# Optimization experiments

Hardware: AMD Instinct MI355X
Metric: run time of the kernel (lower is better)

The kernel has to match this reference:

```python
import jax, jax.numpy as jnp
import numpy as np
from jax import lax

HEADS = 8
C, H, W = 64, 16, 16
D_K = C // HEADS
SCALE = 1.0 / np.sqrt(D_K * H * W).astype(np.float32)


def conv2d(x, w, b):
    # x: [N, C, H, W], w: [O, I, 3, 3], padding=1
    y = lax.conv_general_dilated(x, w, window_strides=(1, 1),
                                 padding=((1, 1), (1, 1)),
                                 dimension_numbers=('NCHW', 'OIHW', 'NCHW'))
    return y + b[None, :, None, None]


def _project(x, w, b, bs, seq):
    # x: [bs, seq, C, H, W] -> conv per frame -> [bs, heads, seq, d_k*H*W]
    y = conv2d(x.reshape(bs * seq, C, H, W), w, b)
    y = y.reshape(bs, seq, HEADS, D_K, H, W)
    y = jnp.transpose(y, (0, 2, 1, 3, 4, 5)).reshape(bs, HEADS, seq, D_K * H * W)
    return y


def setup_inputs() -> dict:
    key = jax.random.key(0)
    ks = jax.random.split(key, 11)
    shp = (2, 256, C, H, W)
    wstd = 1.0 / np.sqrt(C * 9)  # torch Conv2d default init scale
    inp = {
        'q': jax.random.normal(ks[0], shp, jnp.float32),
        'k': jax.random.normal(ks[1], shp, jnp.float32),
        'v': jax.random.normal(ks[2], shp, jnp.float32),
        'Wq': jax.random.uniform(ks[3], (C, C, 3, 3), jnp.float32, -wstd, wstd),
        'bq': jax.random.uniform(ks[4], (C,), jnp.float32, -wstd, wstd),
        'Wk': jax.random.uniform(ks[5], (C, C, 3, 3), jnp.float32, -wstd, wstd),
        'bk': jax.random.uniform(ks[6], (C,), jnp.float32, -wstd, wstd),
        'Wv': jax.random.uniform(ks[7], (C, C, 3, 3), jnp.float32, -wstd, wstd),
        'bv': jax.random.uniform(ks[8], (C,), jnp.float32, -wstd, wstd),
        'Wo': jax.random.uniform(ks[9], (C, C, 3, 3), jnp.float32, -wstd, wstd),
        'bo': jax.random.uniform(ks[10], (C,), jnp.float32, -wstd, wstd),
    }
    return inp


def reference(q, k, v, Wq, bq, Wk, bk, Wv, bv, Wo, bo):
    bs, seq = q.shape[0], q.shape[1]
    qh = _project(q, Wq, bq, bs, seq)  # [bs, h, seq, d_k*H*W]
    kh = _project(k, Wk, bk, bs, seq)
    vh = _project(v, Wv, bv, bs, seq)
    scores = jnp.einsum('bhqd,bhkd->bhqk', qh, kh) * SCALE
    attn = jax.nn.softmax(scores, axis=-1)
    out = jnp.einsum('bhqk,bhkd->bhqd', attn, vh)  # [bs, h, seq, d_k*H*W]
    out = out.reshape(bs, HEADS, seq, D_K, H, W)
    concat = jnp.transpose(out, (0, 2, 1, 3, 4, 5)).reshape(bs * seq, C, H, W)
    y = conv2d(concat, Wo, bo).reshape(bs, seq, C, H, W)
    return y
```

## Files before the change

kernel.cpp:

```cpp
#include <hip/hip_runtime.h>
#include <hip/hip_bf16.h>
#include <hip/hip_fp16.h>

typedef unsigned short u16;
typedef _Float16 f16x8 __attribute__((ext_vector_type(8)));
typedef u16 u16x8 __attribute__((ext_vector_type(8)));
typedef u16 u16x4 __attribute__((ext_vector_type(4)));
typedef float f32x4 __attribute__((ext_vector_type(4)));

__device__ __forceinline__ u16 f2h(float f){
  __half h = __float2half(f);
  return *(u16*)&h;
}

__device__ __forceinline__ void cp16_async(const u16* g, u16* l){
  __builtin_amdgcn_global_load_lds(
      (const __attribute__((address_space(1))) unsigned int*)g,
      (__attribute__((address_space(3))) unsigned int*)l,
      16, 0, 0);
}

__device__ __forceinline__ void prep_w_body(const float* W, u16* Wt, int i){
  if (i >= 36864) return;
  int co = i / 576, rem = i % 576, ci = rem / 9, tap = rem % 9;
  int n = co >> 4, lr = co & 15, kk = ci >> 5, lg = (ci >> 3) & 3, j = ci & 7;
  int s = tap*2 + kk;
  Wt[(((s*4 + n)*64) + lg*16 + lr)*8 + j] = f2h(W[i]);
}

__global__ __launch_bounds__(256) void prep_w3(
    const float* __restrict__ Wq, const float* __restrict__ Wk,
    const float* __restrict__ Wv, u16* __restrict__ Wt)
{
  int which = blockIdx.y;
  const float* W = (which == 0) ? Wq : (which == 1) ? Wk : Wv;
  prep_w_body(W, Wt + which*36864, blockIdx.x * 256 + threadIdx.x);
}

__global__ __launch_bounds__(256) void prep_w(
    const float* __restrict__ W, u16* __restrict__ Wt)
{
  prep_w_body(W, Wt, blockIdx.x * 256 + threadIdx.x);
}

template<bool IN_F32, bool OUT_PROJ>
__device__ __forceinline__ void conv_body(
    const void* __restrict__ xin, const u16* __restrict__ Wt,
    const float* __restrict__ bias, void* __restrict__ dst,
    int frame, u16* xT, int tid)
{
  for (int i = tid; i < 2592; i += 256)
    *(uint4*)((char*)xT + i*16) = make_uint4(0u, 0u, 0u, 0u);
  __syncthreads();

  {
    const int p = tid, py = p >> 4, px = p & 15;
    const int pp = (py + 1)*18 + px + 1;
    const float* xf = (const float*)xin + (size_t)frame * 16384;
    const u16*   xb = (const u16*)  xin + (size_t)frame * 16384;
    #pragma unroll
    for (int cb = 0; cb < 8; ++cb){
      u16x8 pk;
      #pragma unroll
      for (int j = 0; j < 8; ++j){
        int ci = cb*8 + j;
        pk[j] = IN_F32 ? f2h(xf[ci*256 + p]) : xb[ci*256 + p];
      }
      unsigned off = (unsigned)(pp*128) + ((((unsigned)cb + (unsigned)pp) & 7u) << 4);
      *(u16x8*)((char*)xT + off) = pk;
    }
  }
  __syncthreads();

  const int w = tid >> 6, lane = tid & 63, lr = lane & 15, lg = lane >> 4;
  const int pyb = w * 4;

  f32x4 acc[4][4];
  #pragma unroll
  for (int n = 0; n < 4; ++n){
    float b = bias[n*16 + lr];
    #pragma unroll
    for (int m = 0; m < 4; ++m){
      acc[m][n][0] = b; acc[m][n][1] = b; acc[m][n][2] = b; acc[m][n][3] = b;
    }
  }

  #define LOADB(s, B) do {                                                  \
    _Pragma("unroll")                                                       \
    for (int n_ = 0; n_ < 4; ++n_)                                          \
      B[n_] = *(const f16x8*)(Wt + ((((s)*4 + n_)*64) + lane)*8);           \
  } while(0)

  #define STEP(s, B) do {                                                   \
    int tap_ = (s) >> 1, kk_ = (s) & 1;                                     \
    int dy_ = tap_ / 3, dx_ = tap_ - dy_*3;                                 \
    f16x8 af_[4];                                                           \
    _Pragma("unroll")                                                       \
    for (int m_ = 0; m_ < 4; ++m_){                                         \
      int pp_ = (pyb + m_ + dy_)*18 + lr + dx_;                             \
      unsigned slot_ = ((unsigned)(kk_*4 + lg) + (unsigned)pp_) & 7u;       \
      af_[m_] = *(const f16x8*)((const char*)xT                             \
                 + (unsigned)(pp_*128) + (slot_ << 4));                     \
    }                                                                       \
    _Pragma("unroll")                                                       \
    for (int m_ = 0; m_ < 4; ++m_)                                          \
      _Pragma("unroll")                                                     \
      for (int n_ = 0; n_ < 4; ++n_)                                        \
        acc[m_][n_] = __builtin_amdgcn_mfma_f32_16x16x32_f16(               \
            af_[m_], B[n_], acc[m_][n_], 0, 0, 0);                          \
  } while(0)

  f16x8 Ba[4], Bb[4];
  LOADB(0, Ba);
  #pragma unroll 1
  for (int it = 0; it < 9; ++it){
    LOADB(it*2 + 1, Bb);
    STEP(it*2, Ba);
    if (it < 8) LOADB(it*2 + 2, Ba);
    STEP(it*2 + 1, Bb);
  }
  #undef LOADB
  #undef STEP

  __syncthreads();
  char* xTc = (char*)xT;
  if (OUT_PROJ){
    #pragma unroll
    for (int n = 0; n < 4; ++n){
      int co = n*16 + lr;
      #pragma unroll
      for (int m = 0; m < 4; ++m){
        int px0 = w*64 + m*16 + lg*4;
        int s = px0 >> 3;
        unsigned aw = (unsigned)(co*512) + (unsigned)((s ^ (co & 7)) << 4)
                      + (unsigned)((px0 & 7) * 2);
        u16x4 o4;
        #pragma unroll
        for (int r = 0; r < 4; ++r) o4[r] = f2h(acc[m][n][r]);
        *(u16x4*)(xTc + aw) = o4;
      }
    }
    __syncthreads();
    u16* d = (u16*)dst;
    const int b = frame >> 8, sq = frame & 255;
    #pragma unroll
    for (int i = 0; i < 8; ++i){
      int c = w*8 + i;
      int co = c*2 + (lane >> 5);
      int pxo = (lane & 31) * 8;
      unsigned ld = (unsigned)(co*512) + (unsigned)(((lane & 31) ^ (co & 7)) << 4);
      uint4 v = *(const uint4*)(xTc + ld);
      int h = co >> 3, dk = co & 7;
      u16* gp = d + ((size_t)((b*8 + h)*256 + sq))*2048 + dk*256 + pxo;
      *(uint4*)gp = v;
    }
  } else {
    float* dfr = (float*)dst + (size_t)frame * 16384;
    #pragma unroll
    for (int ph2 = 0; ph2 < 2; ++ph2){
      if ((w >> 1) == ph2){
        #pragma unroll
        for (int n = 0; n < 4; ++n){
          int co = n*16 + lr;
          #pragma unroll
          for (int m = 0; m < 4; ++m){
            int pxl = (w & 1)*64 + m*16 + lg*4;
            int s = pxl >> 2;
            unsigned aw = (unsigned)(co*512) + (unsigned)((s ^ (co & 7)) << 4);
            *(f32x4*)(xTc + aw) = acc[m][n];
          }
        }
      }
      __syncthreads();
      #pragma unroll
      for (int i = 0; i < 8; ++i){
        int c = w*8 + i;
        int co = c*2 + (lane >> 5);
        int pxl = (lane & 31) * 4;
        unsigned ld = (unsigned)(co*512) + (unsigned)(((lane & 31) ^ (co & 7)) << 4);
        f32x4 v = *(const f32x4*)(xTc + ld);
        *(f32x4*)(dfr + co*256 + ph2*128 + pxl) = v;
      }
      if (ph2 == 0) __syncthreads();
    }
  }
}

__global__ __launch_bounds__(256, 3) void conv3_mfma(
    const float* __restrict__ q, const float* __restrict__ k,
    const float* __restrict__ v, const u16* __restrict__ Wt3,
    const float* __restrict__ bq, const float* __restrict__ bk,
    const float* __restrict__ bv,
    u16* __restrict__ qh, u16* __restrict__ kh, u16* __restrict__ vh)
{
  __shared__ __align__(16) u16 xT[324 * 64];
  const int which = blockIdx.x >> 9;
  const int frame = blockIdx.x & 511;
  const float* x = (which == 0) ? q : (which == 1) ? k : v;
  const float* bias = (which == 0) ? bq : (which == 1) ? bk : bv;
  u16* dst = (which == 0) ? qh : (which == 1) ? kh : vh;
  conv_body<true, true>(x, Wt3 + which*36864, bias, dst, frame, xT, threadIdx.x);
}

__global__ __launch_bounds__(256, 3) void conv_out_mfma(
    const u16* __restrict__ xin, const u16* __restrict__ Wt,
    const float* __restrict__ bias, float* __restrict__ out)
{
  __shared__ __align__(16) u16 xT[324 * 64];
  conv_body<false, false>(xin, Wt, bias, out, blockIdx.x, xT, threadIdx.x);
}

__global__ __launch_bounds__(256) void transpose_v(
    const u16* __restrict__ vh, u16* __restrict__ vt)
{
  __shared__ u16 tile[64][72];
  const int tid = threadIdx.x;
  const int dt = blockIdx.x, st = blockIdx.y, bh = blockIdx.z;
  {
    int r = tid >> 2, c4 = tid & 3;
    const u16* src = vh + ((size_t)(bh*256 + st*64 + r))*2048 + dt*64 + c4*16;
    uint4 v0 = *(const uint4*)src;
    uint4 v1 = *(const uint4*)(src + 8);
    *(uint4*)&tile[r][c4*16]     = v0;
    *(uint4*)&tile[r][c4*16 + 8] = v1;
  }
  __syncthreads();
  {
    int dr = tid >> 2, s4 = tid & 3;
    u16 tmp[16];
    #pragma unroll
    for (int i = 0; i < 16; ++i) tmp[i] = tile[s4*16 + i][dr];
    u16* dstp = vt + ((size_t)(bh*2048 + dt*64 + dr))*256 + st*64 + s4*16;
    *(uint4*)dstp       = *(uint4*)&tmp[0];
    *(uint4*)(dstp + 8) = *(uint4*)&tmp[8];
  }
}

__global__ __launch_bounds__(512, 2) void attn_kernel(
    const u16* __restrict__ qh, const u16* __restrict__ kh,
    const u16* __restrict__ vt, u16* __restrict__ obuf)
{
  const float SCALE = 0.022097086912079608f;
  __shared__ __align__(16) u16 Qs[16*2048];
  __shared__ __align__(16) u16 Kb[2][16384];
  __shared__ __align__(16) u16 P[16*256];
  __shared__ float redA[8][16];
  __shared__ float redB[8][16];

  const int tid = threadIdx.x;
  const int w = tid >> 6, lane = tid & 63, lr = lane & 15, lg = lane >> 4;

  const int id = blockIdx.x;
  const int xcd = id & 7, j = id >> 3;
  const int bh = xcd + 8*(j & 1), qt = j >> 1;
  const int q0 = qt * 16, b = bh >> 3, h = bh & 7;

  const u16* Qg = qh + ((size_t)(bh*256 + q0))*2048;
  const u16* Kg = kh + (size_t)bh * 256 * 2048;
  const u16* Vg = vt + (size_t)bh * 2048 * 256;

  const int spK = (lane & 7) ^ ((lane >> 3) & 7);
  #define STAGE_K(c, buf)                                                   \
    _Pragma("unroll")                                                       \
    for (int r_ = 0; r_ < 4; ++r_)                                          \
      cp16_async(Kg + (size_t)(w*32 + r_*8 + (lane>>3))*2048 + (c)*64 + spK*8, \
                 (buf) + w*2048 + r_*512);

  #define STAGE_V(c, buf)                                                   \
    _Pragma("unroll")                                                       \
    for (int r_ = 0; r_ < 8; ++r_){                                         \
      int rl_ = w*16 + r_*2 + (lane>>5);                                    \
      int sp_ = (lane & 31) ^ (rl_ & 7);                                    \
      cp16_async(Vg + (size_t)((c)*128 + rl_)*256 + sp_*8,                  \
                 (buf) + w*4096 + r_*512);                                  \
    }

  #pragma unroll
  for (int r = 0; r < 8; ++r){
    int t = r*64 + lane;
    int row = w*2 + (t >> 8);
    int dp = t & 255;
    int sp = (dp & ~7) | ((dp & 7) ^ (row & 7));
    cp16_async(Qg + (size_t)row*2048 + sp*8, Qs + w*4096 + r*512);
  }
  STAGE_K(0, Kb[0]);
  __syncthreads();

  const f32x4 zero4 = {0.f, 0.f, 0.f, 0.f};
  f32x4 sacc[2] = {zero4, zero4};
  #pragma unroll 1
  for (int c = 0; c < 32; ++c){
    if (c < 31) STAGE_K(c+1, Kb[(c+1)&1]);
    const u16* kb = Kb[c&1];
    #pragma unroll
    for (int d2 = 0; d2 < 2; ++d2){
      unsigned aoff = (((unsigned)lr << 12) + (unsigned)(c*128 + d2*64 + lg*16))
                      ^ (unsigned)((lr & 7) << 4);
      f16x8 a = *(const f16x8*)((const char*)Qs + aoff);
      #pragma unroll
      for (int n = 0; n < 2; ++n){
        int row = w*32 + n*16 + lr;
        const u16* kp = kb + row*64 + (((d2*4 + lg) ^ (row & 7)) << 3);
        f16x8 bk = *(const f16x8*)kp;
        sacc[n] = __builtin_amdgcn_mfma_f32_16x16x32_f16(a, bk, sacc[n], 0,0,0);
      }
    }
    __syncthreads();
  }

  float mx[4];
  #pragma unroll
  for (int r = 0; r < 4; ++r){
    float vv = fmaxf(sacc[0][r], sacc[1][r]);
    #pragma unroll
    for (int off = 1; off < 16; off <<= 1) vv = fmaxf(vv, __shfl_xor(vv, off));
    mx[r] = vv;
  }
  if (lr == 0){
    #pragma unroll
    for (int r = 0; r < 4; ++r) redA[w][lg*4 + r] = mx[r];
  }
  __syncthreads();
  #pragma unroll
  for (int r = 0; r < 4; ++r){
    int row = lg*4 + r;
    float vv = redA[0][row];
    #pragma unroll
    for (int ww = 1; ww < 8; ++ww) vv = fmaxf(vv, redA[ww][row]);
    mx[r] = vv;
  }

  const int kbase = w * 32;
  float sm[4] = {0.f, 0.f, 0.f, 0.f};
  #pragma unroll
  for (int n = 0; n < 2; ++n)
    #pragma unroll
    for (int r = 0; r < 4; ++r){
      float pv = __expf((sacc[n][r] - mx[r]) * SCALE);
      sm[r] += pv;
      int row = lg*4 + r;
      int col = kbase + n*16 + lr;
      unsigned off = (((unsigned)row << 9) + ((unsigned)col << 1))
                     ^ (unsigned)((row & 7) << 4);
      *(u16*)((char*)P + off) = f2h(pv);
    }
  #pragma unroll
  for (int r = 0; r < 4; ++r){
    float vv = sm[r];
    #pragma unroll
    for (int off = 1; off < 16; off <<= 1) vv += __shfl_xor(vv, off);
    sm[r] = vv;
  }
  if (lr == 0){
    #pragma unroll
    for (int r = 0; r < 4; ++r) redB[w][lg*4 + r] = sm[r];
  }
  __syncthreads();
  float rs[4];
  #pragma unroll
  for (int r = 0; r < 4; ++r){
    int row = lg*4 + r;
    float s = redB[0][row];
    #pragma unroll
    for (int ww = 1; ww < 8; ++ww) s += redB[ww][row];
    rs[r] = 1.0f / s;
  }

  u16* Vb0 = Qs;
  u16* Vb1 = &Kb[0][0];
  STAGE_V(0, Vb0);
  __syncthreads();
  #pragma unroll 1
  for (int c = 0; c < 16; ++c){
    if (c < 15){
      u16* nbuf = ((c+1) & 1) ? Vb1 : Vb0;
      STAGE_V(c+1, nbuf);
    }
    const u16* vb = (c & 1) ? Vb1 : Vb0;
    f32x4 oacc = zero4;
    #pragma unroll
    for (int kt = 0; kt < 8; ++kt){
      unsigned poff = (((unsigned)lr << 9) + (unsigned)(kt*64 + lg*16))
                      ^ (unsigned)((lr & 7) << 4);
      f16x8 pa = *(const f16x8*)((const char*)P + poff);
      int row = w*16 + lr;
      const u16* vp = vb + row*256 + (((kt*4 + lg) ^ (row & 7)) << 3);
      f16x8 bv = *(const f16x8*)vp;
      oacc = __builtin_amdgcn_mfma_f32_16x16x32_f16(pa, bv, oacc, 0,0,0);
    }
    #pragma unroll
    for (int r = 0; r < 4; ++r){
      float o = oacc[r] * rs[r];
      int qrow = q0 + lg*4 + r;
      int d = c*128 + w*16 + lr;
      int frame = b*256 + qrow;
      int cdim = h*8 + (d >> 8);
      obuf[((size_t)(frame*64 + cdim))*256 + (d & 255)] = f2h(o);
    }
    __syncthreads();
  }
  #undef STAGE_K
  #undef STAGE_V
}

extern "C" void kernel_launch(void* const* d_in, const int* in_sizes, int n_in,
                              void* d_out, int out_size, void* d_ws, size_t ws_size,
                              hipStream_t stream)
{
  const float* q  = (const float*)d_in[0];
  const float* k  = (const float*)d_in[1];
  const float* v  = (const float*)d_in[2];
  const float* Wq = (const float*)d_in[3];
  const float* bq = (const float*)d_in[4];
  const float* Wk = (const float*)d_in[5];
  const float* bk = (const float*)d_in[6];
  const float* Wv = (const float*)d_in[7];
  const float* bv = (const float*)d_in[8];
  const float* Wo = (const float*)d_in[9];
  const float* bo = (const float*)d_in[10];
  float* out = (float*)d_out;

  char* ws = (char*)d_ws;
  u16* qh = (u16*)(ws);
  u16* kh = (u16*)(ws + (size_t)16*1024*1024);
  u16* vh = (u16*)(ws + (size_t)32*1024*1024);
  u16* vt = (u16*)(ws + (size_t)48*1024*1024);
  u16* obuf = vh;
  u16* Wt3  = vt;
  u16* WtO  = qh;

  prep_w3<<<dim3(144, 3), dim3(256), 0, stream>>>(Wq, Wk, Wv, Wt3);
  conv3_mfma<<<dim3(1536), dim3(256), 0, stream>>>(q, k, v, Wt3, bq, bk, bv,
                                                   qh, kh, vh);
  transpose_v<<<dim3(32, 4, 16), dim3(256), 0, stream>>>(vh, vt);
  attn_kernel<<<dim3(256), dim3(512), 0, stream>>>(qh, kh, vt, obuf);
  prep_w<<<dim3(144), dim3(256), 0, stream>>>(Wo, WtO);
  conv_out_mfma<<<dim3(512), dim3(256), 0, stream>>>(obuf, WtO, bo, out);
}
```

Measured before the change: 115.6 us.

## Warp-specialize conv kernels with double-buffered LDS staging across multiple frames

Replaces the one-frame-per-block conv kernels with a persistent 512-thread kernel. Four staging waves load and convert the next frame's input into a second LDS buffer while four compute waves run MFMA on the current frame. Each block handles F frames (6 for the QKV projection, 2 for the output conv), so global-load latency is hidden behind compute. In exchange, LDS per block doubles, half the waves do no MFMA, and the grid shrinks to 256 blocks, which may reduce parallelism across CUs.

```diff
diff --git a/kernel.cpp b/kernel.cpp
--- a/kernel.cpp
+++ b/kernel.cpp
@@ -43,55 +43,79 @@
   prep_w_body(W, Wt, blockIdx.x * 256 + threadIdx.x);
 }
 
-template<bool IN_F32, bool OUT_PROJ>
-__device__ __forceinline__ void conv_body(
-    const void* __restrict__ xin, const u16* __restrict__ Wt,
-    const float* __restrict__ bias, void* __restrict__ dst,
-    int frame, u16* xT, int tid)
+template<bool IN_F32, bool OUT_PROJ, int F>
+__global__ __launch_bounds__(512, 2) void conv_pipe(
+    const void* __restrict__ x0, const void* __restrict__ x1,
+    const void* __restrict__ x2, const u16* __restrict__ Wt_base,
+    int wt_stride, const float* __restrict__ b0,
+    const float* __restrict__ b1, const float* __restrict__ b2,
+    void* __restrict__ d0, void* __restrict__ d1, void* __restrict__ d2)
 {
-  for (int i = tid; i < 2592; i += 256)
-    *(uint4*)((char*)xT + i*16) = make_uint4(0u, 0u, 0u, 0u);
-  __syncthreads();
-
-  {
-    const int p = tid, py = p >> 4, px = p & 15;
-    const int pp = (py + 1)*18 + px + 1;
-    const float* xf = (const float*)xin + (size_t)frame * 16384;
-    const u16*   xb = (const u16*)  xin + (size_t)frame * 16384;
-    #pragma unroll
-    for (int cb = 0; cb < 8; ++cb){
-      u16x8 pk;
-      #pragma unroll
-      for (int j = 0; j < 8; ++j){
-        int ci = cb*8 + j;
-        pk[j] = IN_F32 ? f2h(xf[ci*256 + p]) : xb[ci*256 + p];
-      }
-      unsigned off = (unsigned)(pp*128) + ((((unsigned)cb + (unsigned)pp) & 7u) << 4);
-      *(u16x8*)((char*)xT + off) = pk;
-    }
-  }
-  __syncthreads();
-
+  __shared__ __align__(16) u16 xT0[324*64];
+  __shared__ __align__(16) u16 xT1[324*64];
+  const int tid = threadIdx.x;
   const int w = tid >> 6, lane = tid & 63, lr = lane & 15, lg = lane >> 4;
+  const bool stagew = (w >= 4);
+  const int sp = tid & 255;
+  const int spy = sp >> 4, spx = sp & 15;
+  const int spp = (spy + 1)*18 + spx + 1;
+  const int gf0 = blockIdx.x * F;
   const int pyb = w * 4;
 
-  f32x4 acc[4][4];
-  #pragma unroll
-  for (int n = 0; n < 4; ++n){
-    float b = bias[n*16 + lr];
-    #pragma unroll
-    for (int m = 0; m < 4; ++m){
-      acc[m][n][0] = b; acc[m][n][1] = b; acc[m][n][2] = b; acc[m][n][3] = b;
-    }
-  }
-
-  #define LOADB(s, B) do {                                                  \
+  u16x8 pk[8];
+
+  #define LOADCVT(gf) do {                                                  \
+    int wh_ = (gf) >> 9, fr_ = (gf) & 511;                                  \
+    const void* xs_ = (wh_==0)?x0:(wh_==1)?x1:x2;                           \
+    if (IN_F32){                                                            \
+      const float* s_ = (const float*)xs_ + (size_t)fr_*16384;              \
+      float xv_[64];                                                        \
+      _Pragma("unroll") for (int c=0;c<64;++c) xv_[c] = s_[c*256 + sp];     \
+      _Pragma("unroll") for (int cb=0;cb<8;++cb){                           \
+        u16x8 t_;                                                           \
+        _Pragma("unroll") for (int j=0;j<8;++j) t_[j] = f2h(xv_[cb*8+j]);   \
+        pk[cb] = t_;                                                        \
+      }                                                                     \
+    } else {                                                                \
+      const u16* s_ = (const u16*)xs_ + (size_t)fr_*16384;                  \
+      _Pragma("unroll") for (int cb=0;cb<8;++cb){                           \
+        u16x8 t_;                                                           \
+        _Pragma("unroll") for (int j=0;j<8;++j) t_[j] = s_[(cb*8+j)*256+sp];\
+        pk[cb] = t_;                                                        \
+      }                                                                     \
+    }                                                                       \
+    _Pragma("unroll") for (int cb=0;cb<8;++cb){                             \
+      unsigned* pw_ = (unsigned*)&pk[cb];                                   \
+      asm volatile("" :: "v"(pw_[0]), "v"(pw_[1]), "v"(pw_[2]), "v"(pw_[3]));\
+    }                                                                       \
+  } while(0)
+
+  #define PACKW(buf) do {                                                   \
+    _Pragma("unroll") for (int cb=0;cb<8;++cb){                             \
+      unsigned off_ = (unsigned)(spp*128)                                   \
+                      + ((((unsigned)cb + (unsigned)spp) & 7u) << 4);       \
+      *(u16x8*)((char*)(buf) + off_) = pk[cb];                              \
+    }                                                                       \
+  } while(0)
+
+  #define ZPAD(buf) do {                                                    \
+    for (int i_ = sp; i_ < 544; i_ += 256){                                 \
+      int r_ = i_ >> 3, q_ = i_ & 7, row_;                                  \
+      if (r_ < 18)      row_ = r_;                                          \
+      else if (r_ < 34) row_ = 18*(r_ - 17);                                \
+      else if (r_ < 50) row_ = 18*(r_ - 33) + 17;                           \
+      else              row_ = 306 + (r_ - 50);                             \
+      *(uint4*)((char*)(buf) + row_*128 + q_*16) = make_uint4(0u,0u,0u,0u); \
+    }                                                                       \
+  } while(0)
+
+  #define LOADB(s, B, Wt) do {                                              \
     _Pragma("unroll")                                                       \
     for (int n_ = 0; n_ < 4; ++n_)                                          \
-      B[n_] = *(const f16x8*)(Wt + ((((s)*4 + n_)*64) + lane)*8);           \
+      B[n_] = *(const f16x8*)((Wt) + ((((s)*4 + n_)*64) + lane)*8);         \
   } while(0)
 
-  #define STEP(s, B) do {                                                   \
+  #define STEP(s, B, buf) do {                                              \
     int tap_ = (s) >> 1, kk_ = (s) & 1;                                     \
     int dy_ = tap_ / 3, dx_ = tap_ - dy_*3;                                 \
     f16x8 af_[4];                                                           \
@@ -99,7 +123,7 @@
     for (int m_ = 0; m_ < 4; ++m_){                                         \
       int pp_ = (pyb + m_ + dy_)*18 + lr + dx_;                             \
       unsigned slot_ = ((unsigned)(kk_*4 + lg) + (unsigned)pp_) & 7u;       \
-      af_[m_] = *(const f16x8*)((const char*)xT                             \
+      af_[m_] = *(const f16x8*)((const char*)(buf)                          \
                  + (unsigned)(pp_*128) + (slot_ << 4));                     \
     }                                                                       \
     _Pragma("unroll")                                                       \
@@ -110,55 +134,89 @@
             af_[m_], B[n_], acc[m_][n_], 0, 0, 0);                          \
   } while(0)
 
-  f16x8 Ba[4], Bb[4];
-  LOADB(0, Ba);
+  if (stagew) LOADCVT(gf0);
+  for (int i = tid; i < 2592; i += 512){
+    *(uint4*)((char*)xT0 + i*16) = make_uint4(0u,0u,0u,0u);
+    *(uint4*)((char*)xT1 + i*16) = make_uint4(0u,0u,0u,0u);
+  }
+  __syncthreads();
+  if (stagew) PACKW(xT0);
+  __syncthreads();
+
   #pragma unroll 1
-  for (int it = 0; it < 9; ++it){
-    LOADB(it*2 + 1, Bb);
-    STEP(it*2, Ba);
-    if (it < 8) LOADB(it*2 + 2, Ba);
-    STEP(it*2 + 1, Bb);
-  }
-  #undef LOADB
-  #undef STEP
-
-  __syncthreads();
-  char* xTc = (char*)xT;
-  if (OUT_PROJ){
-    #pragma unroll
-    for (int n = 0; n < 4; ++n){
-      int co = n*16 + lr;
+  for (int f = 0; f < F; ++f){
+    const int gf = gf0 + f;
+    const int wh = gf >> 9, frame = gf & 511;
+    const u16* Wt = Wt_base + wh*wt_stride;
+    const float* bias = (wh==0)?b0:(wh==1)?b1:b2;
+    u16* cur = (f & 1) ? xT1 : xT0;
+    u16* nxt = (f & 1) ? xT0 : xT1;
+
+    if (stagew && f + 1 < F) LOADCVT(gf + 1);
+
+    f32x4 acc[4][4];
+    if (!stagew){
       #pragma unroll
-      for (int m = 0; m < 4; ++m){
-        int px0 = w*64 + m*16 + lg*4;
-        int s = px0 >> 3;
-        unsigned aw = (unsigned)(co*512) + (unsigned)((s ^ (co & 7)) << 4)
-                      + (unsigned)((px0 & 7) * 2);
-        u16x4 o4;
-        #pragma unroll
-        for (int r = 0; r < 4; ++r) o4[r] = f2h(acc[m][n][r]);
-        *(u16x4*)(xTc + aw) = o4;
+      for (int n = 0; n < 4; ++n){
+        float b = bias[n*16 + lr];
+        #pragma unroll
+        for (int m = 0; m < 4; ++m){
+          acc[m][n][0] = b; acc[m][n][1] = b; acc[m][n][2] = b; acc[m][n][3] = b;
+        }
+      }
+      f16x8 Ba[4], Bb[4];
+      LOADB(0, Ba, Wt);
+      #pragma unroll 1
+      for (int it = 0; it < 9; ++it){
+        LOADB(it*2 + 1, Bb, Wt);
+        STEP(it*2, Ba, cur);
+        if (it < 8) LOADB(it*2 + 2, Ba, Wt);
+        STEP(it*2 + 1, Bb, cur);
       }
     }
     __syncthreads();
-    u16* d = (u16*)dst;
-    const int b = frame >> 8, sq = frame & 255;
-    #pragma unroll
-    for (int i = 0; i < 8; ++i){
-      int c = w*8 + i;
-      int co = c*2 + (lane >> 5);
-      int pxo = (lane & 31) * 8;
-      unsigned ld = (unsigned)(co*512) + (unsigned)(((lane & 31) ^ (co & 7)) << 4);
-      uint4 v = *(const uint4*)(xTc + ld);
-      int h = co >> 3, dk = co & 7;
-      u16* gp = d + ((size_t)((b*8 + h)*256 + sq))*2048 + dk*256 + pxo;
-      *(uint4*)gp = v;
-    }
-  } else {
-    float* dfr = (float*)dst + (size_t)frame * 16384;
-    #pragma unroll
-    for (int ph2 = 0; ph2 < 2; ++ph2){
-      if ((w >> 1) == ph2){
+
+    char* tc = (char*)cur;
+    if (OUT_PROJ){
+      if (!stagew){
+        #pragma unroll
+        for (int n = 0; n < 4; ++n){
+          int co = n*16 + lr;
+          #pragma unroll
+          for (int m = 0; m < 4; ++m){
+            int px0 = w*64 + m*16 + lg*4;
+            int s = px0 >> 3;
+            unsigned aw = (unsigned)(co*512) + (unsigned)((s ^ (co & 7)) << 4)
+                          + (unsigned)((px0 & 7) * 2);
+            u16x4 o4;
+            #pragma unroll
+            for (int r = 0; r < 4; ++r) o4[r] = f2h(acc[m][n][r]);
+            *(u16x4*)(tc + aw) = o4;
+          }
+        }
+      } else if (f + 1 < F){
+        ZPAD(nxt); PACKW(nxt);
+      }
+      __syncthreads();
+      if (!stagew){
+        u16* d = (u16*)((wh==0)?d0:(wh==1)?d1:d2);
+        const int b = frame >> 8, sq = frame & 255;
+        #pragma unroll
+        for (int i = 0; i < 8; ++i){
+          int c = w*8 + i;
+          int co = c*2 + (lane >> 5);
+          int pxo = (lane & 31) * 8;
+          unsigned ld = (unsigned)(co*512) + (unsigned)(((lane & 31) ^ (co & 7)) << 4);
+          uint4 v = *(const uint4*)(tc + ld);
+          int h = co >> 3, dk = co & 7;
+          u16* gp = d + ((size_t)((b*8 + h)*256 + sq))*2048 + dk*256 + pxo;
+          *(uint4*)gp = v;
+        }
+      }
+      __syncthreads();
+    } else {
+      float* dfr = (float*)d0 + (size_t)frame * 16384;
+      if (!stagew && (w >> 1) == 0){
         #pragma unroll
         for (int n = 0; n < 4; ++n){
           int co = n*16 + lr;
@@ -167,47 +225,57 @@
             int pxl = (w & 1)*64 + m*16 + lg*4;
             int s = pxl >> 2;
             unsigned aw = (unsigned)(co*512) + (unsigned)((s ^ (co & 7)) << 4);
-            *(f32x4*)(xTc + aw) = acc[m][n];
+            *(f32x4*)(tc + aw) = acc[m][n];
           }
         }
       }
+      if (stagew && f + 1 < F){ ZPAD(nxt); PACKW(nxt); }
       __syncthreads();
-      #pragma unroll
-      for (int i = 0; i < 8; ++i){
-        int c = w*8 + i;
-        int co = c*2 + (lane >> 5);
-        int pxl = (lane & 31) * 4;
-        unsigned ld = (unsigned)(co*512) + (unsigned)(((lane & 31) ^ (co & 7)) << 4);
-        f32x4 v = *(const f32x4*)(xTc + ld);
-        *(f32x4*)(dfr + co*256 + ph2*128 + pxl) = v;
-      }
-      if (ph2 == 0) __syncthreads();
-    }
-  }
-}
-
-__global__ __launch_bounds__(256, 3) void conv3_mfma(
-    const float* __restrict__ q, const float* __restrict__ k,
-    const float* __restrict__ v, const u16* __restrict__ Wt3,
-    const float* __restrict__ bq, const float* __restrict__ bk,
-    const float* __restrict__ bv,
-    u16* __restrict__ qh, u16* __restrict__ kh, u16* __restrict__ vh)
-{
-  __shared__ __align__(16) u16 xT[324 * 64];
-  const int which = blockIdx.x >> 9;
-  const int frame = blockIdx.x & 511;
-  const float* x = (which == 0) ? q : (which == 1) ? k : v;
-  const float* bias = (which == 0) ? bq : (which == 1) ? bk : bv;
-  u16* dst = (which == 0) ? qh : (which == 1) ? kh : vh;
-  conv_body<true, true>(x, Wt3 + which*36864, bias, dst, frame, xT, threadIdx.x);
-}
-
-__global__ __launch_bounds__(256, 3) void conv_out_mfma(
-    const u16* __restrict__ xin, const u16* __restrict__ Wt,
-    const float* __restrict__ bias, float* __restrict__ out)
-{
-  __shared__ __align__(16) u16 xT[324 * 64];
-  conv_body<false, false>(xin, Wt, bias, out, blockIdx.x, xT, threadIdx.x);
+      if (!stagew){
+        #pragma unroll
+        for (int i = 0; i < 8; ++i){
+          int c = w*8 + i;
+          int co = c*2 + (lane >> 5);
+          int pxl = (lane & 31) * 4;
+          unsigned ld = (unsigned)(co*512) + (unsigned)(((lane & 31) ^ (co & 7)) << 4);
+          f32x4 v = *(const f32x4*)(tc + ld);
+          *(f32x4*)(dfr + co*256 + pxl) = v;
+        }
+      }
+      __syncthreads();
+      if (!stagew && (w >> 1) == 1){
+        #pragma unroll
+        for (int n = 0; n < 4; ++n){
+          int co = n*16 + lr;
+          #pragma unroll
+          for (int m = 0; m < 4; ++m){
+            int pxl = (w & 1)*64 + m*16 + lg*4;
+            int s = pxl >> 2;
+            unsigned aw = (unsigned)(co*512) + (unsigned)((s ^ (co & 7)) << 4);
+            *(f32x4*)(tc + aw) = acc[m][n];
+          }
+        }
+      }
+      __syncthreads();
+      if (!stagew){
+        #pragma unroll
+        for (int i = 0; i < 8; ++i){
+          int c = w*8 + i;
+          int co = c*2 + (lane >> 5);
+          int pxl = (lane & 31) * 4;
+          unsigned ld = (unsigned)(co*512) + (unsigned)(((lane & 31) ^ (co & 7)) << 4);
+          f32x4 v = *(const f32x4*)(tc + ld);
+          *(f32x4*)(dfr + co*256 + 128 + pxl) = v;
+        }
+      }
+      __syncthreads();
+    }
+  }
+  #undef LOADCVT
+  #undef PACKW
+  #undef ZPAD
+  #undef LOADB
+  #undef STEP
 }
 
 __global__ __launch_bounds__(256) void transpose_v(
@@ -430,10 +498,11 @@
   u16* WtO  = qh;
 
   prep_w3<<<dim3(144, 3), dim3(256), 0, stream>>>(Wq, Wk, Wv, Wt3);
-  conv3_mfma<<<dim3(1536), dim3(256), 0, stream>>>(q, k, v, Wt3, bq, bk, bv,
-                                                   qh, kh, vh);
+  conv_pipe<true, true, 6><<<dim3(256), dim3(512), 0, stream>>>(
+      q, k, v, Wt3, 36864, bq, bk, bv, qh, kh, vh);
   transpose_v<<<dim3(32, 4, 16), dim3(256), 0, stream>>>(vh, vt);
   attn_kernel<<<dim3(256), dim3(512), 0, stream>>>(qh, kh, vt, obuf);
   prep_w<<<dim3(144), dim3(256), 0, stream>>>(Wo, WtO);
-  conv_out_mfma<<<dim3(512), dim3(256), 0, stream>>>(obuf, WtO, bo, out);
-}
+  conv_pipe<false, false, 2><<<dim3(256), dim3(512), 0, stream>>>(
+      obuf, obuf, obuf, WtO, 0, bo, bo, bo, out, out, out);
+}
```

Result: slower. 132.8 us (+14.8%).
